# Performance work log

Measured on AMD Instinct MI355X. Metric: run time of the kernel, lower is better.

Reference implementation:

```python
import jax, jax.numpy as jnp
import numpy as np

N = 100000   # nodes (src == dst count)
E = 800000   # edges
D = 64       # hidden_dim == out_channels per head
H = 4        # heads
ED = 2       # edge_dim
NEG_SLOPE = 0.2
EPS = 1e-16


def setup_inputs() -> dict:
    key = jax.random.key(0)
    ks = jax.random.split(key, 12)
    s = 1.0 / np.sqrt(D)
    return {
        "x_src": jax.random.normal(ks[0], (N, D), jnp.float32),
        "x_dst": jax.random.normal(ks[1], (N, D), jnp.float32),
        "edge_index": jax.random.randint(ks[2], (2, E), 0, N),
        "edge_attr": jax.random.normal(ks[3], (E, ED), jnp.float32),
        "gamma": jnp.ones((D,), jnp.float32),
        "beta": jnp.zeros((D,), jnp.float32),
        "W_l": jax.random.normal(ks[4], (D, H * D), jnp.float32) * s,
        "b_l": jnp.zeros((H * D,), jnp.float32),
        "W_r": jax.random.normal(ks[5], (D, H * D), jnp.float32) * s,
        "b_r": jnp.zeros((H * D,), jnp.float32),
        "W_e": jax.random.normal(ks[6], (ED, H * D), jnp.float32) * s,
        "att": jax.random.normal(ks[7], (H, D), jnp.float32) * s,
        "bias": jnp.zeros((D,), jnp.float32),
    }


def _layernorm(x, gamma, beta):
    mu = jnp.mean(x, axis=-1, keepdims=True)
    var = jnp.var(x, axis=-1, keepdims=True)
    return (x - mu) * jax.lax.rsqrt(var + 1e-5) * gamma + beta


def reference(x_src, x_dst, edge_index, edge_attr, gamma, beta,
              W_l, b_l, W_r, b_r, W_e, att, bias):
    # shared LayerNorm on both bipartite node sets
    xs = _layernorm(x_src, gamma, beta)
    xd = _layernorm(x_dst, gamma, beta)
    # per-node linear transforms -> [N, H, D]
    hl = (xs @ W_l + b_l).reshape(N, H, D)   # source transform
    hr = (xd @ W_r + b_r).reshape(N, H, D)   # destination transform
    he = (edge_attr @ W_e).reshape(E, H, D)  # edge transform (no bias)
    src, dst = edge_index[0], edge_index[1]
    # GATv2 score: LeakyReLU(x_j + x_i + e) . att
    m = jax.nn.leaky_relu(hl[src] + hr[dst] + he, NEG_SLOPE)  # [E, H, D]
    alpha = jnp.einsum('ehd,hd->eh', m, att)                  # [E, H]
    # segment softmax over edges sharing a destination
    amax = jax.ops.segment_max(alpha, dst, num_segments=N)    # [N, H]
    ex = jnp.exp(alpha - amax[dst])
    denom = jax.ops.segment_sum(ex, dst, num_segments=N)      # [N, H]
    alpha = ex / (denom[dst] + EPS)
    # scatter-aggregate messages x_j * alpha
    out = jax.ops.segment_sum(hl[src] * alpha[..., None], dst, num_segments=N)  # [N, H, D]
    # concat=False -> mean over heads, then bias
    return out.mean(axis=1) + bias
```

## Files before the change

kernel.cpp:

```cpp
#include <hip/hip_runtime.h>
#include <hip/hip_bf16.h>
#include <cstdint>

#define NN 100000
#define EE 800000
#define DD 64
#define HH 4
#define HDIM 256
#define NEG 0.2f
#define L2E 1.4426950408889634f
#define CAP 44
#define HLMASK 0x03FFFFF8

#define NGB ((NN + 63) / 64)
#define GEMM_BLOCKS (NGB * 2)
#define SCAT_BLOCKS ((EE + 255) / 256)
#define SCAT4_BLOCKS ((EE + 1023) / 1024)
#define TOTAL_BLOCKS (SCAT4_BLOCKS * 5)

typedef __attribute__((ext_vector_type(8))) short bf16x8;
typedef __attribute__((ext_vector_type(4))) float f32x4;
typedef __attribute__((ext_vector_type(2))) float f32x2;

__device__ __forceinline__ float bf2f(unsigned short u) {
  union { unsigned int i; float f; } c; c.i = ((unsigned int)u) << 16; return c.f;
}
__device__ __forceinline__ unsigned short f2bf(float f) {
  union { float f; unsigned int i; } c; c.f = f;
  unsigned int r = c.i + 0x7FFF + ((c.i >> 16) & 1);
  return (unsigned short)(r >> 16);
}
__device__ __forceinline__ unsigned int pack2(unsigned short a, unsigned short b) {
  return (unsigned int)a | ((unsigned int)b << 16);
}
__device__ __forceinline__ f32x2 unpk(unsigned int u) {
  union { unsigned int i; float f; } lo, hi;
  lo.i = u << 16; hi.i = u & 0xffff0000u;
  f32x2 r; r.x = lo.f; r.y = hi.f; return r;
}
__device__ __forceinline__ f32x2 abs2(f32x2 a) {
  f32x2 r; r.x = fmaxf(a.x, -a.x); r.y = fmaxf(a.y, -a.y); return r;
}

#if __has_builtin(__builtin_amdgcn_exp2f)
#define EXP2F(x) __builtin_amdgcn_exp2f(x)
#else
#define EXP2F(x) exp2f(x)
#endif

#define ROWSUM16(p) do {                                                         \
  p += __int_as_float(__builtin_amdgcn_update_dpp(0, __float_as_int(p), 0x121, 0xF, 0xF, false)); \
  p += __int_as_float(__builtin_amdgcn_update_dpp(0, __float_as_int(p), 0x122, 0xF, 0xF, false)); \
  p += __int_as_float(__builtin_amdgcn_update_dpp(0, __float_as_int(p), 0x124, 0xF, 0xF, false)); \
  p += __int_as_float(__builtin_amdgcn_update_dpp(0, __float_as_int(p), 0x128, 0xF, 0xF, false)); \
} while (0)

#define CIDX(l) ((((l) >> 4) << 6) + (((l) & 3) << 4) + ((((l) >> 2) & 3) << 2))

__device__ __forceinline__ void prep_body(
    int mat,
    const float* __restrict__ W_l, const float* __restrict__ b_l,
    const float* __restrict__ W_r, const float* __restrict__ b_r,
    const float* __restrict__ gamma, const float* __restrict__ beta,
    unsigned short* __restrict__ Wgt, float* __restrict__ cw,
    float* __restrict__ cb)
{
  const int c = threadIdx.x;
  const float* W = mat ? W_r : W_l;
  const float* bb = mat ? b_r : b_l;
  unsigned short* wout = Wgt + (size_t)mat * HDIM * DD + (size_t)c * DD;
  float s_cw = 0.f, s_cb = 0.f;
#pragma unroll 8
  for (int k = 0; k < DD; ++k) {
    float wv = W[k * HDIM + c];
    unsigned short u = f2bf(gamma[k] * wv);
    wout[k] = u;
    s_cw += bf2f(u);
    s_cb += beta[k] * wv;
  }
  cw[mat * HDIM + c] = s_cw;
  cb[mat * HDIM + c] = s_cb + bb[c];
}

__global__ __launch_bounds__(256) void k_prep(
    const float* __restrict__ W_l, const float* __restrict__ b_l,
    const float* __restrict__ W_r, const float* __restrict__ b_r,
    const float* __restrict__ gamma, const float* __restrict__ beta,
    unsigned short* __restrict__ Wgt, float* __restrict__ cw,
    float* __restrict__ cb, int* __restrict__ deg)
{
  if (blockIdx.x < 2) {
    prep_body(blockIdx.x, W_l, b_l, W_r, b_r, gamma, beta, Wgt, cw, cb);
    return;
  }
  int i = (blockIdx.x - 2) * 256 + threadIdx.x;
  if (i < NN) deg[i] = 0;
}

__device__ __forceinline__ void gemm_body(
    int gx,
    const float* __restrict__ x_src, const float* __restrict__ x_dst,
    const unsigned short* __restrict__ Wgt, const float* __restrict__ cw,
    const float* __restrict__ cb,
    unsigned short* __restrict__ hl, unsigned short* __restrict__ hr)
{
  const int mat = gx & 1;
  const int tile = gx >> 1;
  const int t = threadIdx.x;
  const float* __restrict__ xp = mat ? x_dst : x_src;
  unsigned short* __restrict__ HM = mat ? hr : hl;

  __shared__ __align__(16) unsigned short sh[2][64 * 72];
  __shared__ float smu[64], sinv[64];

  const int l = t & 63, w = t >> 6;
  const int row16 = l & 15, hq = l >> 4;
  const int c0 = w * 64;

  const int sr = t >> 2, sq = t & 3;
  float v[16];
  {
    const int n = tile * 64 + sr;
    if (n < NN) {
      const f32x4* xr = (const f32x4*)(xp + (size_t)n * DD + sq * 16);
#pragma unroll
      for (int j = 0; j < 4; ++j) {
        f32x4 f = __builtin_nontemporal_load(xr + j);
        v[4 * j + 0] = f.x; v[4 * j + 1] = f.y;
        v[4 * j + 2] = f.z; v[4 * j + 3] = f.w;
      }
    } else {
#pragma unroll
      for (int j = 0; j < 16; ++j) v[j] = 0.f;
    }
  }

  const unsigned short* WgtM = Wgt + (size_t)mat * HDIM * DD;
  bf16x8 bfr[4][2];
#pragma unroll
  for (int cbk = 0; cbk < 4; ++cbk)
#pragma unroll
    for (int kb = 0; kb < 2; ++kb)
      bfr[cbk][kb] = *(const bf16x8*)(WgtM + (size_t)(c0 + cbk * 16 + row16) * DD
                                      + kb * 32 + hq * 8);
  float4 cw4[4], cb4[4];
#pragma unroll
  for (int cbk = 0; cbk < 4; ++cbk) {
    cw4[cbk] = *(const float4*)(cw + mat * HDIM + c0 + cbk * 16 + hq * 4);
    cb4[cbk] = *(const float4*)(cb + mat * HDIM + c0 + cbk * 16 + hq * 4);
  }

  {
    float s = 0.f, s2 = 0.f;
#pragma unroll
    for (int j = 0; j < 16; ++j) { s += v[j]; s2 += v[j] * v[j]; }
    s  += __shfl_xor(s, 1, 64);  s  += __shfl_xor(s, 2, 64);
    s2 += __shfl_xor(s2, 1, 64); s2 += __shfl_xor(s2, 2, 64);
    const float mu = s * (1.0f / DD);
    const float var = s2 * (1.0f / DD) - mu * mu;
    const float inv = rsqrtf(var + 1e-5f);
    if (sq == 0) { smu[sr] = mu; sinv[sr] = inv; }
    unsigned short hi[16], lo[16];
#pragma unroll
    for (int j = 0; j < 16; ++j) {
      unsigned short h = f2bf(v[j]);
      hi[j] = h;
      lo[j] = f2bf(v[j] - bf2f(h));
    }
    const int base = sr * 72 + sq * 16;
    uint4 w0, w1;
    w0.x = pack2(hi[0], hi[1]);  w0.y = pack2(hi[2], hi[3]);
    w0.z = pack2(hi[4], hi[5]);  w0.w = pack2(hi[6], hi[7]);
    w1.x = pack2(hi[8], hi[9]);  w1.y = pack2(hi[10], hi[11]);
    w1.z = pack2(hi[12], hi[13]); w1.w = pack2(hi[14], hi[15]);
    *(uint4*)(&sh[0][base]) = w0;
    *(uint4*)(&sh[0][base + 8]) = w1;
    w0.x = pack2(lo[0], lo[1]);  w0.y = pack2(lo[2], lo[3]);
    w0.z = pack2(lo[4], lo[5]);  w0.w = pack2(lo[6], lo[7]);
    w1.x = pack2(lo[8], lo[9]);  w1.y = pack2(lo[10], lo[11]);
    w1.z = pack2(lo[12], lo[13]); w1.w = pack2(lo[14], lo[15]);
    *(uint4*)(&sh[1][base]) = w0;
    *(uint4*)(&sh[1][base + 8]) = w1;
  }
  __syncthreads();

#pragma unroll
  for (int rb = 0; rb < 4; ++rb) {
    const int abase = (rb * 16 + row16) * 72 + hq * 8;
    bf16x8 xh0 = *(const bf16x8*)(&sh[0][abase]);
    bf16x8 xh1 = *(const bf16x8*)(&sh[0][abase + 32]);
    bf16x8 xl0 = *(const bf16x8*)(&sh[1][abase]);
    bf16x8 xl1 = *(const bf16x8*)(&sh[1][abase + 32]);
    f32x4 acc[4];
#pragma unroll
    for (int cbk = 0; cbk < 4; ++cbk) {
      acc[cbk] = (f32x4){0.f, 0.f, 0.f, 0.f};
      acc[cbk] = __builtin_amdgcn_mfma_f32_16x16x32_bf16(bfr[cbk][0], xh0, acc[cbk], 0, 0, 0);
      acc[cbk] = __builtin_amdgcn_mfma_f32_16x16x32_bf16(bfr[cbk][1], xh1, acc[cbk], 0, 0, 0);
      acc[cbk] = __builtin_amdgcn_mfma_f32_16x16x32_bf16(bfr[cbk][0], xl0, acc[cbk], 0, 0, 0);
      acc[cbk] = __builtin_amdgcn_mfma_f32_16x16x32_bf16(bfr[cbk][1], xl1, acc[cbk], 0, 0, 0);
    }
    const int nloc = rb * 16 + row16;
    const int node = tile * 64 + nloc;
    const float mu = smu[nloc], inv = sinv[nloc];
    if (node < NN) {
      float hh[4][4];
#pragma unroll
      for (int cbk = 0; cbk < 4; ++cbk) {
        hh[cbk][0] = fmaf(-mu, cw4[cbk].x, acc[cbk][0]) * inv + cb4[cbk].x;
        hh[cbk][1] = fmaf(-mu, cw4[cbk].y, acc[cbk][1]) * inv + cb4[cbk].y;
        hh[cbk][2] = fmaf(-mu, cw4[cbk].z, acc[cbk][2]) * inv + cb4[cbk].z;
        hh[cbk][3] = fmaf(-mu, cw4[cbk].w, acc[cbk][3]) * inv + cb4[cbk].w;
      }
      unsigned short* rp = HM + (size_t)node * HDIM + c0 + hq * 16;
      uint4 s0, s1;
      s0.x = pack2(f2bf(hh[0][0]), f2bf(hh[0][1]));
      s0.y = pack2(f2bf(hh[0][2]), f2bf(hh[0][3]));
      s0.z = pack2(f2bf(hh[1][0]), f2bf(hh[1][1]));
      s0.w = pack2(f2bf(hh[1][2]), f2bf(hh[1][3]));
      s1.x = pack2(f2bf(hh[2][0]), f2bf(hh[2][1]));
      s1.y = pack2(f2bf(hh[2][2]), f2bf(hh[2][3]));
      s1.z = pack2(f2bf(hh[3][0]), f2bf(hh[3][1]));
      s1.w = pack2(f2bf(hh[3][2]), f2bf(hh[3][3]));
      *(uint4*)rp = s0;
      *(uint4*)(rp + 8) = s1;
    }
  }
}

__device__ __forceinline__ void scatter_body4(
    int bx, const int* __restrict__ ei, const float* __restrict__ eattr,
    int* __restrict__ deg, int2* __restrict__ epack)
{
  const int e0 = bx * 1024 + threadIdx.x;
  int src[4], dst[4];
  unsigned long long ea[4];
  bool ok[4];
#pragma unroll
  for (int k = 0; k < 4; ++k) {
    const int e = e0 + k * 256;
    ok[k] = (e < EE);
    const int es = ok[k] ? e : 0;
    src[k] = __builtin_nontemporal_load(ei + es);
    dst[k] = __builtin_nontemporal_load(ei + EE + es);
    ea[k]  = __builtin_nontemporal_load((const unsigned long long*)(eattr + 2 * es));
  }
  int slot[4];
#pragma unroll
  for (int k = 0; k < 4; ++k) {
    if (ok[k]) slot[k] = atomicAdd(&deg[dst[k]], 1);
    else slot[k] = CAP;
  }
#pragma unroll
  for (int k = 0; k < 4; ++k) {
    if (slot[k] < CAP) {
      const float eax = __uint_as_float((unsigned int)ea[k]);
      const float eay = __uint_as_float((unsigned int)(ea[k] >> 32));
      unsigned long long rec =
          (unsigned long long)(unsigned int)(src[k] << 9)
          | ((unsigned long long)pack2(f2bf(eax), f2bf(eay)) << 32);
      __builtin_nontemporal_store(
          rec, (unsigned long long*)(epack + (size_t)dst[k] * CAP + slot[k]));
    }
  }
}

__global__ __launch_bounds__(256) void k_gemm_scatter(
    const float* __restrict__ x_src, const float* __restrict__ x_dst,
    const unsigned short* __restrict__ Wgt, const float* __restrict__ cw,
    const float* __restrict__ cb,
    unsigned short* __restrict__ hl, unsigned short* __restrict__ hr,
    const int* __restrict__ ei, const float* __restrict__ eattr,
    int* __restrict__ deg, int2* __restrict__ epack)
{
  const int bx = blockIdx.x;
  const int q = bx / 5, r = bx - q * 5;
  if (r == 4) {
    scatter_body4(q, ei, eattr, deg, epack);
  } else {
    const int g = q * 4 + r;
    if (g < GEMM_BLOCKS)
      gemm_body(g, x_src, x_dst, Wgt, cw, cb, hl, hr);
  }
}

__global__ __launch_bounds__(256, 8) void k_agg(
    const int* __restrict__ deg,
    const unsigned short* __restrict__ hl, const unsigned short* __restrict__ hr,
    const float* __restrict__ W_e, const float* __restrict__ att,
    const float* __restrict__ bias, const int2* __restrict__ epack,
    float* __restrict__ out)
{
  const int t = threadIdx.x;
  const int l = t & 63;
  const int loff = l * 8;
  const int cidx = CIDX(l);
  const char* hlb = (const char*)hl;

  const float4 at4 = *(const float4*)(att + cidx);
  const float4 w0  = *(const float4*)(W_e + cidx);
  const float4 w1  = *(const float4*)(W_e + HDIM + cidx);
  f32x2 atA01, atA23, atB01, atB23, w001, w023, w101, w123;
  atA01.x = at4.x * (0.6f * L2E); atA01.y = at4.y * (0.6f * L2E);
  atA23.x = at4.z * (0.6f * L2E); atA23.y = at4.w * (0.6f * L2E);
  atB01.x = at4.x * (0.4f * L2E); atB01.y = at4.y * (0.4f * L2E);
  atB23.x = at4.z * (0.4f * L2E); atB23.y = at4.w * (0.4f * L2E);
  w001.x = w0.x; w001.y = w0.y; w023.x = w0.z; w023.y = w0.w;
  w101.x = w1.x; w101.y = w1.y; w123.x = w1.z; w123.y = w1.w;

  const int nwaves = gridDim.x * (blockDim.x >> 6);
  const int wid0 = blockIdx.x * (blockDim.x >> 6) + (t >> 6);
  if (wid0 >= NN) return;

  int pdeg = 0;
  {
    const int pn = wid0 + l * nwaves;
    if (pn < NN) pdeg = deg[pn];
  }

  int it = 0;
  for (int n = wid0; n < NN; n += nwaves, ++it) {
    const int nu = __builtin_amdgcn_readfirstlane(n);
    const int cnt = min(__shfl(pdeg, it), CAP);
    const unsigned long long hvv = __builtin_nontemporal_load(
        (const unsigned long long*)(hr + (size_t)nu * HDIM + l * 4));
    const f32x2 r01 = unpk((unsigned int)hvv), r23 = unpk((unsigned int)(hvv >> 32));
    f32x2 acc01 = {0.f, 0.f}, acc23 = {0.f, 0.f};
    float den = 0.f;

    auto EDGE = [&](int ey, uint2 av) {
      const f32x2 eav = unpk((unsigned int)ey);
      const f32x2 a01 = unpk(av.x), a23 = unpk(av.y);
      f32x2 s01 = a01 + r01 + w001 * eav.x + w101 * eav.y;
      f32x2 s23 = a23 + r23 + w023 * eav.x + w123 * eav.y;
      f32x2 q = s01 * atA01 + abs2(s01) * atB01;
      q = q + s23 * atA23 + abs2(s23) * atB23;
      float p = q.x + q.y;
      ROWSUM16(p);
      const float ex = EXP2F(p);
      acc01 += a01 * ex;
      acc23 += a23 * ex;
      den += ex;
    };

    if (cnt > 0) {
      const int2* eptr = epack + (size_t)nu * CAP;
      int2 e0 = eptr[0], e1 = eptr[1], e2 = eptr[2], e3 = eptr[3],
           e4 = eptr[4], e5 = eptr[5], e6 = eptr[6], e7 = eptr[7];
      uint2 a0 = *(const uint2*)(hlb + (e0.x & HLMASK) + loff);
      uint2 a1 = *(const uint2*)(hlb + (e1.x & HLMASK) + loff);
      uint2 a2 = *(const uint2*)(hlb + (e2.x & HLMASK) + loff);
      uint2 a3 = *(const uint2*)(hlb + (e3.x & HLMASK) + loff);
      int i = 0;
      for (; i + 4 <= cnt; i += 4) {
        uint2 b4 = *(const uint2*)(hlb + ((i + 4 < cnt) ? (e4.x & HLMASK) : 0) + loff);
        uint2 b5 = *(const uint2*)(hlb + ((i + 5 < cnt) ? (e5.x & HLMASK) : 0) + loff);
        uint2 b6 = *(const uint2*)(hlb + ((i + 6 < cnt) ? (e6.x & HLMASK) : 0) + loff);
        uint2 b7 = *(const uint2*)(hlb + ((i + 7 < cnt) ? (e7.x & HLMASK) : 0) + loff);
        int2 t0 = eptr[i + 8], t1 = eptr[i + 9],
             t2 = eptr[i + 10], t3 = eptr[i + 11];
        EDGE(e0.y, a0);
        EDGE(e1.y, a1);
        EDGE(e2.y, a2);
        EDGE(e3.y, a3);
        e0 = e4; e1 = e5; e2 = e6; e3 = e7;
        e4 = t0; e5 = t1; e6 = t2; e7 = t3;
        a0 = b4; a1 = b5; a2 = b6; a3 = b7;
      }
      const int rem = cnt - i;
      if (rem > 0) EDGE(e0.y, a0);
      if (rem > 1) EDGE(e1.y, a1);
      if (rem > 2) EDGE(e2.y, a2);
    }

    const float inv = 1.0f / (den + 1e-16f);
    float v0 = acc01.x * inv, v1 = acc01.y * inv;
    float v2 = acc23.x * inv, v3 = acc23.y * inv;
    v0 += __shfl_xor(v0, 16, 64); v0 += __shfl_xor(v0, 32, 64);
    v1 += __shfl_xor(v1, 16, 64); v1 += __shfl_xor(v1, 32, 64);
    v2 += __shfl_xor(v2, 16, 64); v2 += __shfl_xor(v2, 32, 64);
    v3 += __shfl_xor(v3, 16, 64); v3 += __shfl_xor(v3, 32, 64);
    if (l < 16) {
      const float4 bias4 = *(const float4*)(bias + cidx);
      f32x4 o;
      o.x = 0.25f * v0 + bias4.x;
      o.y = 0.25f * v1 + bias4.y;
      o.z = 0.25f * v2 + bias4.z;
      o.w = 0.25f * v3 + bias4.w;
      __builtin_nontemporal_store(o, (f32x4*)(out + (size_t)nu * DD + cidx));
    }
  }
}

__global__ __launch_bounds__(256) void k_prep_count(
    const float* __restrict__ W_l, const float* __restrict__ b_l,
    const float* __restrict__ W_r, const float* __restrict__ b_r,
    const float* __restrict__ gamma, const float* __restrict__ beta,
    unsigned short* __restrict__ Wgt, float* __restrict__ cw,
    float* __restrict__ cb,
    const int* __restrict__ ei, int* __restrict__ counts)
{
  if (blockIdx.x < 2) {
    prep_body(blockIdx.x, W_l, b_l, W_r, b_r, gamma, beta, Wgt, cw, cb);
  } else {
    int e = (blockIdx.x - 2) * 256 + threadIdx.x;
    if (e < EE) atomicAdd(&counts[ei[EE + e]], 1);
  }
}

__global__ __launch_bounds__(256) void k_base(const int* __restrict__ counts,
                                              int* __restrict__ cursor,
                                              int* __restrict__ rowstart,
                                              int* __restrict__ cur) {
  const int lane = threadIdx.x & 63;
  const int wid = (blockIdx.x * blockDim.x + threadIdx.x) >> 6;
  const int n = wid * 64 + lane;
  int val = (n < NN) ? counts[n] : 0;
  int s = val;
#pragma unroll
  for (int off = 1; off < 64; off <<= 1) {
    int tsh = __shfl_up(s, off, 64);
    if (lane >= off) s += tsh;
  }
  int total = __shfl(s, 63, 64);
  int base = 0;
  if (lane == 0) base = atomicAdd(cursor, total);
  base = __shfl(base, 0, 64);
  if (n < NN) {
    int rs = base + s - val;
    rowstart[n] = rs;
    cur[n] = rs;
  }
}

__global__ __launch_bounds__(256) void k_scatter_csr(const int* __restrict__ ei,
                                                     const float* __restrict__ eattr,
                                                     int* __restrict__ cur,
                                                     int2* __restrict__ epack) {
  int e = blockIdx.x * blockDim.x + threadIdx.x;
  if (e >= EE) return;
  if (e < 64) epack[EE + e] = make_int2(0, 0);
  int src = ei[e];
  int dst = ei[EE + e];
  float2 ea = *(const float2*)(eattr + 2 * e);
  int pos = atomicAdd(&cur[dst], 1);
  epack[pos] = make_int2(src << 9, (int)pack2(f2bf(ea.x), f2bf(ea.y)));
}

__global__ __launch_bounds__(256, 8) void k_agg_csr(
    const int* __restrict__ rowstart, const int* __restrict__ counts,
    const unsigned short* __restrict__ hl, const unsigned short* __restrict__ hr,
    const float* __restrict__ W_e, const float* __restrict__ att,
    const float* __restrict__ bias, const int2* __restrict__ epack,
    float* __restrict__ out)
{
  const int t = threadIdx.x;
  const int l = t & 63;
  const int loff = l * 8;
  const int cidx = CIDX(l);
  const char* hlb = (const char*)hl;
  const float4 at4 = *(const float4*)(att + cidx);
  const float4 w0  = *(const float4*)(W_e + cidx);
  const float4 w1  = *(const float4*)(W_e + HDIM + cidx);
  f32x2 atA01, atA23, atB01, atB23, w001, w023, w101, w123;
  atA01.x = at4.x * (0.6f * L2E); atA01.y = at4.y * (0.6f * L2E);
  atA23.x = at4.z * (0.6f * L2E); atA23.y = at4.w * (0.6f * L2E);
  atB01.x = at4.x * (0.4f * L2E); atB01.y = at4.y * (0.4f * L2E);
  atB23.x = at4.z * (0.4f * L2E); atB23.y = at4.w * (0.4f * L2E);
  w001.x = w0.x; w001.y = w0.y; w023.x = w0.z; w023.y = w0.w;
  w101.x = w1.x; w101.y = w1.y; w123.x = w1.z; w123.y = w1.w;
  const int nwaves = gridDim.x * (blockDim.x >> 6);
  const int wid0 = blockIdx.x * (blockDim.x >> 6) + (t >> 6);
  for (int n = wid0; n < NN; n += nwaves) {
    const int nu = __builtin_amdgcn_readfirstlane(n);
    const int start = __builtin_amdgcn_readfirstlane(rowstart[nu]);
    const int cnt = __builtin_amdgcn_readfirstlane(counts[nu]);
    const uint2 hv = *(const uint2*)(hr + (size_t)nu * HDIM + l * 4);
    const f32x2 r01 = unpk(hv.x), r23 = unpk(hv.y);
    f32x2 acc01 = {0.f, 0.f}, acc23 = {0.f, 0.f};
    float den = 0.f;
    for (int i = 0; i < cnt; ++i) {
      int2 ep = epack[start + i];
      uint2 av = *(const uint2*)(hlb + (ep.x & HLMASK) + loff);
      const f32x2 eav = unpk((unsigned int)ep.y);
      const f32x2 a01 = unpk(av.x), a23 = unpk(av.y);
      f32x2 s01 = a01 + r01 + w001 * eav.x + w101 * eav.y;
      f32x2 s23 = a23 + r23 + w023 * eav.x + w123 * eav.y;
      f32x2 q = s01 * atA01 + abs2(s01) * atB01;
      q = q + s23 * atA23 + abs2(s23) * atB23;
      float p = q.x + q.y;
      ROWSUM16(p);
      const float ex = EXP2F(p);
      acc01 += a01 * ex;
      acc23 += a23 * ex;
      den += ex;
    }
    const float inv = 1.0f / (den + 1e-16f);
    float v0 = acc01.x * inv, v1 = acc01.y * inv;
    float v2 = acc23.x * inv, v3 = acc23.y * inv;
    v0 += __shfl_xor(v0, 16, 64); v0 += __shfl_xor(v0, 32, 64);
    v1 += __shfl_xor(v1, 16, 64); v1 += __shfl_xor(v1, 32, 64);
    v2 += __shfl_xor(v2, 16, 64); v2 += __shfl_xor(v2, 32, 64);
    v3 += __shfl_xor(v3, 16, 64); v3 += __shfl_xor(v3, 32, 64);
    if (l < 16) {
      const float4 bias4 = *(const float4*)(bias + cidx);
      float4 o;
      o.x = 0.25f * v0 + bias4.x;
      o.y = 0.25f * v1 + bias4.y;
      o.z = 0.25f * v2 + bias4.z;
      o.w = 0.25f * v3 + bias4.w;
      *(float4*)(out + (size_t)nu * DD + cidx) = o;
    }
  }
}

__global__ __launch_bounds__(256) void k_gemm_only(
    const float* __restrict__ x_src, const float* __restrict__ x_dst,
    const unsigned short* __restrict__ Wgt, const float* __restrict__ cw,
    const float* __restrict__ cb,
    unsigned short* __restrict__ hl, unsigned short* __restrict__ hr)
{
  gemm_body(blockIdx.x, x_src, x_dst, Wgt, cw, cb, hl, hr);
}

extern "C" void kernel_launch(void* const* d_in, const int* in_sizes, int n_in,
                              void* d_out, int out_size, void* d_ws, size_t ws_size,
                              hipStream_t stream) {
  const float* x_src = (const float*)d_in[0];
  const float* x_dst = (const float*)d_in[1];
  const int*   ei    = (const int*)d_in[2];
  const float* eattr = (const float*)d_in[3];
  const float* gamma = (const float*)d_in[4];
  const float* beta  = (const float*)d_in[5];
  const float* W_l   = (const float*)d_in[6];
  const float* b_l   = (const float*)d_in[7];
  const float* W_r   = (const float*)d_in[8];
  const float* b_r   = (const float*)d_in[9];
  const float* W_e   = (const float*)d_in[10];
  const float* att   = (const float*)d_in[11];
  const float* bias  = (const float*)d_in[12];
  float* out = (float*)d_out;

  char* ws = (char*)d_ws;
  unsigned short* hl = (unsigned short*)ws;
  unsigned short* hr = hl + (size_t)NN * HDIM;
  char* rest = (char*)(hr + (size_t)NN * HDIM);

  const size_t fixed_need = (size_t)NN * HDIM * 2 * 2
                          + ((size_t)NN * CAP + 64) * 8
                          + 2 * HDIM * DD * 2 + 4 * HDIM * 4
                          + (size_t)NN * 4 + 4096;

  if (ws_size >= fixed_need) {
    int2* epack = (int2*)rest;
    unsigned short* Wgt = (unsigned short*)(epack + (size_t)NN * CAP + 64);
    float* cw = (float*)(Wgt + 2 * HDIM * DD);
    float* cb = cw + 2 * HDIM;
    int* deg = (int*)(cb + 2 * HDIM);

    k_prep<<<2 + (NN + 255) / 256, 256, 0, stream>>>(
        W_l, b_l, W_r, b_r, gamma, beta, Wgt, cw, cb, deg);
    k_gemm_scatter<<<TOTAL_BLOCKS, 256, 0, stream>>>(
        x_src, x_dst, Wgt, cw, cb, hl, hr, ei, eattr, deg, epack);
    k_agg<<<2048, 256, 0, stream>>>(deg, hl, hr, W_e, att, bias, epack, out);
  } else {
    int2* epack = (int2*)rest;
    unsigned short* Wgt = (unsigned short*)(epack + EE + 64);
    float* cw = (float*)(Wgt + 2 * HDIM * DD);
    float* cb = cw + 2 * HDIM;
    int* counts   = (int*)(cb + 2 * HDIM);
    int* cursor   = counts + NN;
    int* rowstart = cursor + 1;
    int* cur      = rowstart + NN;

    hipMemsetAsync(counts, 0, (size_t)(NN + 1) * sizeof(int), stream);
    k_prep_count<<<2 + SCAT_BLOCKS, 256, 0, stream>>>(
        W_l, b_l, W_r, b_r, gamma, beta, Wgt, cw, cb, ei, counts);
    k_base<<<(NGB * 64 + 255) / 256, 256, 0, stream>>>(
        counts, cursor, rowstart, cur);
    k_gemm_only<<<GEMM_BLOCKS, 256, 0, stream>>>(
        x_src, x_dst, Wgt, cw, cb, hl, hr);
    k_scatter_csr<<<SCAT_BLOCKS, 256, 0, stream>>>(ei, eattr, cur, epack);
    k_agg_csr<<<2048, 256, 0, stream>>>(rowstart, counts, hl, hr, W_e, att,
                                        bias, epack, out);
  }
}
```

Measured before the change: 154.4 us.

## Process two edges per wave with 16-byte half-wave gathers in aggregation

Restructures the aggregation kernel so each half-wave (32 lanes) handles a different edge, and each lane loads 16 bytes (8 bf16) of the source row instead of 8 bytes. The per-edge score reduction shrinks to 3 shuffles within 8-lane groups, and the two half-wave accumulators are combined once at the end. Masking by edge index replaces the scalar remainder tail. LeakyReLU now uses fmax instead of the abs-decomposition, and launch bounds drop to 4 waves per SIMD. This adds register pressure and wasted lanes for odd-degree nodes.

```diff
diff --git a/kernel.cpp b/kernel.cpp
--- a/kernel.cpp
+++ b/kernel.cpp
@@ -11,6 +11,7 @@
 #define L2E 1.4426950408889634f
 #define CAP 44
 #define HLMASK 0x03FFFFF8
+#define ROWMASK 0x03FFFE00
 
 #define NGB ((NN + 63) / 64)
 #define GEMM_BLOCKS (NGB * 2)
@@ -21,6 +22,7 @@
 typedef __attribute__((ext_vector_type(8))) short bf16x8;
 typedef __attribute__((ext_vector_type(4))) float f32x4;
 typedef __attribute__((ext_vector_type(2))) float f32x2;
+typedef __attribute__((ext_vector_type(4))) unsigned int u32x4;
 
 __device__ __forceinline__ float bf2f(unsigned short u) {
   union { unsigned int i; float f; } c; c.i = ((unsigned int)u) << 16; return c.f;
@@ -284,7 +286,7 @@
   }
 }
 
-__global__ __launch_bounds__(256, 8) void k_agg(
+__global__ __launch_bounds__(256, 4) void k_agg(
     const int* __restrict__ deg,
     const unsigned short* __restrict__ hl, const unsigned short* __restrict__ hr,
     const float* __restrict__ W_e, const float* __restrict__ att,
@@ -293,20 +295,32 @@
 {
   const int t = threadIdx.x;
   const int l = t & 63;
-  const int loff = l * 8;
-  const int cidx = CIDX(l);
+  const int half = (l >> 5) & 1;
+  const int sl = l & 31;
+  const int goff = sl * 16;
   const char* hlb = (const char*)hl;
 
-  const float4 at4 = *(const float4*)(att + cidx);
-  const float4 w0  = *(const float4*)(W_e + cidx);
-  const float4 w1  = *(const float4*)(W_e + HDIM + cidx);
-  f32x2 atA01, atA23, atB01, atB23, w001, w023, w101, w123;
-  atA01.x = at4.x * (0.6f * L2E); atA01.y = at4.y * (0.6f * L2E);
-  atA23.x = at4.z * (0.6f * L2E); atA23.y = at4.w * (0.6f * L2E);
-  atB01.x = at4.x * (0.4f * L2E); atB01.y = at4.y * (0.4f * L2E);
-  atB23.x = at4.z * (0.4f * L2E); atB23.y = at4.w * (0.4f * L2E);
-  w001.x = w0.x; w001.y = w0.y; w023.x = w0.z; w023.y = w0.w;
-  w101.x = w1.x; w101.y = w1.y; w123.x = w1.z; w123.y = w1.w;
+  const int headc = (sl >> 3) << 6;
+  const int hq4 = ((sl >> 1) & 3) << 2;
+  const int idxA = headc + (((2 * sl) & 3) << 4) + hq4;
+  const int idxB = headc + (((2 * sl + 1) & 3) << 4) + hq4;
+
+  const float4 aA = *(const float4*)(att + idxA);
+  const float4 aB = *(const float4*)(att + idxB);
+  f32x2 at0, at1, at2, at3;
+  at0.x = aA.x * L2E; at0.y = aA.y * L2E;
+  at1.x = aA.z * L2E; at1.y = aA.w * L2E;
+  at2.x = aB.x * L2E; at2.y = aB.y * L2E;
+  at3.x = aB.z * L2E; at3.y = aB.w * L2E;
+  const float4 w0A = *(const float4*)(W_e + idxA);
+  const float4 w0B = *(const float4*)(W_e + idxB);
+  const float4 w1A = *(const float4*)(W_e + HDIM + idxA);
+  const float4 w1B = *(const float4*)(W_e + HDIM + idxB);
+  f32x2 w00, w01, w02, w03, w10, w11, w12, w13;
+  w00.x = w0A.x; w00.y = w0A.y; w01.x = w0A.z; w01.y = w0A.w;
+  w02.x = w0B.x; w02.y = w0B.y; w03.x = w0B.z; w03.y = w0B.w;
+  w10.x = w1A.x; w10.y = w1A.y; w11.x = w1A.z; w11.y = w1A.w;
+  w12.x = w1B.x; w12.y = w1B.y; w13.x = w1B.z; w13.y = w1B.w;
 
   const int nwaves = gridDim.x * (blockDim.x >> 6);
   const int wid0 = blockIdx.x * (blockDim.x >> 6) + (t >> 6);
@@ -322,72 +336,79 @@
   for (int n = wid0; n < NN; n += nwaves, ++it) {
     const int nu = __builtin_amdgcn_readfirstlane(n);
     const int cnt = min(__shfl(pdeg, it), CAP);
-    const unsigned long long hvv = __builtin_nontemporal_load(
-        (const unsigned long long*)(hr + (size_t)nu * HDIM + l * 4));
-    const f32x2 r01 = unpk((unsigned int)hvv), r23 = unpk((unsigned int)(hvv >> 32));
-    f32x2 acc01 = {0.f, 0.f}, acc23 = {0.f, 0.f};
+    const u32x4 hv = __builtin_nontemporal_load(
+        (const u32x4*)((const char*)hr + (size_t)nu * (HDIM * 2) + goff));
+    const f32x2 r0 = unpk(hv.x), r1 = unpk(hv.y), r2 = unpk(hv.z), r3 = unpk(hv.w);
+    f32x2 acc0 = {0.f, 0.f}, acc1 = {0.f, 0.f}, acc2 = {0.f, 0.f}, acc3 = {0.f, 0.f};
     float den = 0.f;
 
-    auto EDGE = [&](int ey, uint2 av) {
-      const f32x2 eav = unpk((unsigned int)ey);
-      const f32x2 a01 = unpk(av.x), a23 = unpk(av.y);
-      f32x2 s01 = a01 + r01 + w001 * eav.x + w101 * eav.y;
-      f32x2 s23 = a23 + r23 + w023 * eav.x + w123 * eav.y;
-      f32x2 q = s01 * atA01 + abs2(s01) * atB01;
-      q = q + s23 * atA23 + abs2(s23) * atB23;
+    auto EDGE2 = [&](int gy, uint4 av, int eidx) {
+      const f32x2 eav = unpk((unsigned int)gy);
+      const f32x2 a_0 = unpk(av.x), a_1 = unpk(av.y), a_2 = unpk(av.z), a_3 = unpk(av.w);
+      f32x2 s0 = a_0 + r0 + w00 * eav.x + w10 * eav.y;
+      f32x2 s1 = a_1 + r1 + w01 * eav.x + w11 * eav.y;
+      f32x2 s2 = a_2 + r2 + w02 * eav.x + w12 * eav.y;
+      f32x2 s3 = a_3 + r3 + w03 * eav.x + w13 * eav.y;
+      f32x2 m0, m1, m2, m3;
+      m0.x = fmaxf(s0.x, 0.2f * s0.x); m0.y = fmaxf(s0.y, 0.2f * s0.y);
+      m1.x = fmaxf(s1.x, 0.2f * s1.x); m1.y = fmaxf(s1.y, 0.2f * s1.y);
+      m2.x = fmaxf(s2.x, 0.2f * s2.x); m2.y = fmaxf(s2.y, 0.2f * s2.y);
+      m3.x = fmaxf(s3.x, 0.2f * s3.x); m3.y = fmaxf(s3.y, 0.2f * s3.y);
+      f32x2 q = m0 * at0;
+      q = q + m1 * at1;
+      q = q + m2 * at2;
+      q = q + m3 * at3;
       float p = q.x + q.y;
-      ROWSUM16(p);
-      const float ex = EXP2F(p);
-      acc01 += a01 * ex;
-      acc23 += a23 * ex;
+      p += __shfl_xor(p, 1, 64);
+      p += __shfl_xor(p, 2, 64);
+      p += __shfl_xor(p, 4, 64);
+      float ex = EXP2F(p);
+      ex = ((eidx + half) < cnt) ? ex : 0.f;
+      acc0 += a_0 * ex; acc1 += a_1 * ex;
+      acc2 += a_2 * ex; acc3 += a_3 * ex;
       den += ex;
     };
 
     if (cnt > 0) {
-      const int2* eptr = epack + (size_t)nu * CAP;
-      int2 e0 = eptr[0], e1 = eptr[1], e2 = eptr[2], e3 = eptr[3],
-           e4 = eptr[4], e5 = eptr[5], e6 = eptr[6], e7 = eptr[7];
-      uint2 a0 = *(const uint2*)(hlb + (e0.x & HLMASK) + loff);
-      uint2 a1 = *(const uint2*)(hlb + (e1.x & HLMASK) + loff);
-      uint2 a2 = *(const uint2*)(hlb + (e2.x & HLMASK) + loff);
-      uint2 a3 = *(const uint2*)(hlb + (e3.x & HLMASK) + loff);
-      int i = 0;
-      for (; i + 4 <= cnt; i += 4) {
-        uint2 b4 = *(const uint2*)(hlb + ((i + 4 < cnt) ? (e4.x & HLMASK) : 0) + loff);
-        uint2 b5 = *(const uint2*)(hlb + ((i + 5 < cnt) ? (e5.x & HLMASK) : 0) + loff);
-        uint2 b6 = *(const uint2*)(hlb + ((i + 6 < cnt) ? (e6.x & HLMASK) : 0) + loff);
-        uint2 b7 = *(const uint2*)(hlb + ((i + 7 < cnt) ? (e7.x & HLMASK) : 0) + loff);
-        int2 t0 = eptr[i + 8], t1 = eptr[i + 9],
-             t2 = eptr[i + 10], t3 = eptr[i + 11];
-        EDGE(e0.y, a0);
-        EDGE(e1.y, a1);
-        EDGE(e2.y, a2);
-        EDGE(e3.y, a3);
-        e0 = e4; e1 = e5; e2 = e6; e3 = e7;
-        e4 = t0; e5 = t1; e6 = t2; e7 = t3;
-        a0 = b4; a1 = b5; a2 = b6; a3 = b7;
+      const int2* eptr = epack + (size_t)nu * CAP + half;
+      int2 g0 = eptr[0], g1 = eptr[2], g2 = eptr[4], g3 = eptr[6];
+      uint4 a0 = *(const uint4*)(hlb + ((0 + half < cnt) ? (g0.x & ROWMASK) : 0) + goff);
+      uint4 a1 = *(const uint4*)(hlb + ((2 + half < cnt) ? (g1.x & ROWMASK) : 0) + goff);
+      for (int i = 0; i < cnt; i += 4) {
+        uint4 b2 = *(const uint4*)(hlb + ((i + 4 + half < cnt) ? (g2.x & ROWMASK) : 0) + goff);
+        uint4 b3 = *(const uint4*)(hlb + ((i + 6 + half < cnt) ? (g3.x & ROWMASK) : 0) + goff);
+        int2 t0 = eptr[i + 8], t1 = eptr[i + 10];
+        EDGE2(g0.y, a0, i);
+        EDGE2(g1.y, a1, i + 2);
+        g0 = g2; g1 = g3; g2 = t0; g3 = t1;
+        a0 = b2; a1 = b3;
       }
-      const int rem = cnt - i;
-      if (rem > 0) EDGE(e0.y, a0);
-      if (rem > 1) EDGE(e1.y, a1);
-      if (rem > 2) EDGE(e2.y, a2);
-    }
-
-    const float inv = 1.0f / (den + 1e-16f);
-    float v0 = acc01.x * inv, v1 = acc01.y * inv;
-    float v2 = acc23.x * inv, v3 = acc23.y * inv;
-    v0 += __shfl_xor(v0, 16, 64); v0 += __shfl_xor(v0, 32, 64);
-    v1 += __shfl_xor(v1, 16, 64); v1 += __shfl_xor(v1, 32, 64);
-    v2 += __shfl_xor(v2, 16, 64); v2 += __shfl_xor(v2, 32, 64);
-    v3 += __shfl_xor(v3, 16, 64); v3 += __shfl_xor(v3, 32, 64);
-    if (l < 16) {
-      const float4 bias4 = *(const float4*)(bias + cidx);
-      f32x4 o;
-      o.x = 0.25f * v0 + bias4.x;
-      o.y = 0.25f * v1 + bias4.y;
-      o.z = 0.25f * v2 + bias4.z;
-      o.w = 0.25f * v3 + bias4.w;
-      __builtin_nontemporal_store(o, (f32x4*)(out + (size_t)nu * DD + cidx));
+    }
+
+    den += __shfl_xor(den, 32, 64);
+    acc0.x += __shfl_xor(acc0.x, 32, 64); acc0.y += __shfl_xor(acc0.y, 32, 64);
+    acc1.x += __shfl_xor(acc1.x, 32, 64); acc1.y += __shfl_xor(acc1.y, 32, 64);
+    acc2.x += __shfl_xor(acc2.x, 32, 64); acc2.y += __shfl_xor(acc2.y, 32, 64);
+    acc3.x += __shfl_xor(acc3.x, 32, 64); acc3.y += __shfl_xor(acc3.y, 32, 64);
+    const float inv = 0.25f / (den + 1e-16f);
+    float v0 = acc0.x * inv, v1 = acc0.y * inv, v2 = acc1.x * inv, v3 = acc1.y * inv;
+    float v4 = acc2.x * inv, v5 = acc2.y * inv, v6 = acc3.x * inv, v7 = acc3.y * inv;
+    v0 += __shfl_xor(v0, 8, 64);  v0 += __shfl_xor(v0, 16, 64);
+    v1 += __shfl_xor(v1, 8, 64);  v1 += __shfl_xor(v1, 16, 64);
+    v2 += __shfl_xor(v2, 8, 64);  v2 += __shfl_xor(v2, 16, 64);
+    v3 += __shfl_xor(v3, 8, 64);  v3 += __shfl_xor(v3, 16, 64);
+    v4 += __shfl_xor(v4, 8, 64);  v4 += __shfl_xor(v4, 16, 64);
+    v5 += __shfl_xor(v5, 8, 64);  v5 += __shfl_xor(v5, 16, 64);
+    v6 += __shfl_xor(v6, 8, 64);  v6 += __shfl_xor(v6, 16, 64);
+    v7 += __shfl_xor(v7, 8, 64);  v7 += __shfl_xor(v7, 16, 64);
+    if (l < 8) {
+      const float4 bA = *(const float4*)(bias + idxA);
+      const float4 bB = *(const float4*)(bias + idxB);
+      f32x4 oA, oB;
+      oA.x = v0 + bA.x; oA.y = v1 + bA.y; oA.z = v2 + bA.z; oA.w = v3 + bA.w;
+      oB.x = v4 + bB.x; oB.y = v5 + bB.y; oB.z = v6 + bB.z; oB.w = v7 + bB.w;
+      __builtin_nontemporal_store(oA, (f32x4*)(out + (size_t)nu * DD + idxA));
+      __builtin_nontemporal_store(oB, (f32x4*)(out + (size_t)nu * DD + idxB));
     }
   }
 }
```

Measured after the change: 185.6 us. +20.2%, slower.
